# Performance work log

Hardware: AMD Instinct MI355X
Metric: run time of the kernel (lower is better)

## Reference

```python
import jax, jax.numpy as jnp
import numpy as np

N_NODE = 50000
EMB = 128
LAYERS = 2
B = 1024
L = 50
E = 1_600_000


def setup_inputs() -> dict:
    key = jax.random.key(0)
    ks = jax.random.split(key, 21)
    d = EMB
    stdv = 1.0 / np.sqrt(d)
    u = lambda k, shape: jax.random.uniform(k, shape, minval=-stdv, maxval=stdv, dtype=jnp.float32)
    inp = {
        'adj_row': jax.random.randint(ks[0], (E,), 0, N_NODE, dtype=jnp.int32),
        'adj_col': jax.random.randint(ks[1], (E,), 0, N_NODE, dtype=jnp.int32),
        'adj_val': jax.random.uniform(ks[2], (E,), dtype=jnp.float32) / 32.0,  # ~row-normalized sparse adjacency
        'embedding': jax.random.normal(ks[3], (N_NODE, d), dtype=jnp.float32) * 0.1,
        'session_item': jax.random.randint(ks[4], (B, L), 0, N_NODE, dtype=jnp.int32),  # 0 hits the zero pad row
        'session_len': jnp.full((B, 1), float(L), dtype=jnp.float32),
        'D': jax.random.uniform(ks[5], (B, B), dtype=jnp.float32) / B,
        'A_sess': jax.random.uniform(ks[6], (B, B), dtype=jnp.float32) / B,
        'A_gnn': jax.random.uniform(ks[7], (B, L, 2 * L), dtype=jnp.float32) / L,
        'alias_pos': jax.random.randint(ks[8], (B, L), 0, L, dtype=jnp.int32),
        'hidden': jax.random.normal(ks[9], (B, L, d), dtype=jnp.float32) * 0.1,
        'W_in': u(ks[10], (d, d)), 'b_in': u(ks[11], (d,)),
        'W_out': u(ks[12], (d, d)), 'b_out': u(ks[13], (d,)),
        'w_ih': u(ks[14], (3 * d, 2 * d)), 'b_ih': u(ks[15], (3 * d,)),
        'w_hh': u(ks[16], (3 * d, d)), 'b_hh': u(ks[17], (3 * d,)),
        'b_iah': u(ks[18], (d,)), 'b_oah': u(ks[19], (d,)),
    }
    return inp


def reference(adj_row, adj_col, adj_val, embedding, session_item, session_len,
              D, A_sess, A_gnn, alias_pos, hidden,
              W_in, b_in, W_out, b_out, w_ih, b_ih, w_hh, b_hh, b_iah, b_oah):
    # ---- HyperConv: layers of sparse (COO) adjacency @ embedding, summed over hops ----
    emb = embedding
    final = embedding
    for _ in range(LAYERS):
        emb = jax.ops.segment_sum(adj_val[:, None] * emb[adj_col], adj_row, num_segments=N_NODE)
        final = final + emb
    item_emb = final  # [N_NODE, d]

    # ---- LineConv: zero-padded gather + mean pool over session, then session-graph propagation ----
    pad_table = jnp.concatenate([jnp.zeros((1, EMB), embedding.dtype), embedding], axis=0)
    seq_h = pad_table[session_item]                      # [B, L, d]
    sess = jnp.sum(seq_h, axis=1) / session_len          # [B, d]
    DA = D @ A_sess                                      # [B, B]
    acc = sess
    s = sess
    for _ in range(LAYERS):
        s = DA @ s
        acc = acc + s
    session_emb = acc                                    # [B, d]

    # ---- GNN: gather per-session in/out adjacency rows, gated GRU-style update ----
    in_out = jnp.take_along_axis(A_gnn, alias_pos[:, :, None], axis=1)  # [B, L, 2L]
    h_in = hidden @ W_in.T + b_in
    h_out = hidden @ W_out.T + b_out
    input_in = jnp.einsum('bij,bjd->bid', in_out[:, :, :L], h_in) + b_iah
    input_out = jnp.einsum('bij,bjd->bid', in_out[:, :, L:], h_out) + b_oah
    inputs = jnp.concatenate([input_in, input_out], axis=2)             # [B, L, 2d]
    gi = inputs @ w_ih.T + b_ih
    gh = hidden @ w_hh.T + b_hh
    i_r, i_i, i_n = jnp.split(gi, 3, axis=2)
    h_r, h_i, h_n = jnp.split(gh, 3, axis=2)
    resetgate = jax.nn.sigmoid(i_r + h_r)
    inputgate = jax.nn.sigmoid(i_i + h_i)
    newgate = jnp.tanh(i_n + resetgate * h_n)
    hy = newgate + inputgate * (hidden - newgate)        # [B, L, d]

    return item_emb, session_emb, hy
```

## Files before the change

### kernel.cpp

```cpp
#include <hip/hip_runtime.h>

#define EMB 128
#define NN 50000
#define BB 1024
#define LL 50
#define NBK 49
#define NEB 512

typedef float f32x4 __attribute__((ext_vector_type(4)));
typedef float f32x2 __attribute__((ext_vector_type(2)));
typedef unsigned short u16;
typedef unsigned int u32;
typedef unsigned long long u64;
typedef u16 u16x4 __attribute__((ext_vector_type(4)));
typedef u32 u32x4 __attribute__((ext_vector_type(4)));
typedef short bf16x8 __attribute__((ext_vector_type(8)));

__device__ __forceinline__ float u2f(u16 u) {
    union { unsigned int i; float f; } v; v.i = ((unsigned int)u) << 16; return v.f;
}
__device__ __forceinline__ u16 f2b(float f) {
    union { float f; unsigned int i; } v; v.f = f;
    unsigned int i = v.i;
    return (u16)((i + 0x7FFFu + ((i >> 16) & 1u)) >> 16);
}
__device__ __forceinline__ float lo2f(u32 w) { return u2f((u16)(w & 0xffffu)); }
__device__ __forceinline__ float hi2f(u32 w) { return u2f((u16)(w >> 16)); }
__device__ __forceinline__ float sigmoidf_(float x) { return 1.f / (1.f + __expf(-x)); }

__device__ __forceinline__ bf16x8 ld_cvt8(const float* p) {
    f32x4 v0 = *(const f32x4*)p;
    f32x4 v1 = *(const f32x4*)(p + 4);
    union { u16 u[8]; bf16x8 b; } r;
#pragma unroll
    for (int t = 0; t < 4; t++) { r.u[t] = f2b(v0[t]); r.u[4 + t] = f2b(v1[t]); }
    return r.b;
}

__global__ __launch_bounds__(256) void prep_kernel(
    const float* __restrict__ emb, const float* __restrict__ A, const float* __restrict__ D,
    const float* __restrict__ wih, const float* __restrict__ whh,
    const float* __restrict__ Win, const float* __restrict__ Wout,
    u16* __restrict__ emb_bf, u16* __restrict__ A_bf, u16* __restrict__ D_bf,
    u16* __restrict__ wih_bf, u16* __restrict__ whh_bf,
    u16* __restrict__ Win_bf, u16* __restrict__ Wout_bf,
    const int* __restrict__ rowi, int* __restrict__ bcnt,
    int E, int chunk)
{
    __shared__ int lc[NBK];
    int gid = blockIdx.x * 256 + threadIdx.x;
    int stride = gridDim.x * 256;
    int tid = threadIdx.x;
    if (blockIdx.x < NEB) {
        if (tid < NBK) lc[tid] = 0;
        __syncthreads();
        int beg = blockIdx.x * chunk, end = min(E, beg + chunk);
        for (int e = beg + tid; e < end; e += 256)
            atomicAdd(&lc[rowi[e] >> 10], 1);
        __syncthreads();
        if (tid < NBK) bcnt[blockIdx.x * NBK + tid] = lc[tid];
    }
    for (int i = gid; i < 1600000; i += stride) {
        f32x4 v = *(const f32x4*)(emb + (size_t)i * 4);
        u16x4 p;
#pragma unroll
        for (int t = 0; t < 4; t++) p[t] = f2b(v[t]);
        *(u16x4*)(emb_bf + (size_t)i * 4) = p;
    }
    for (int i = gid; i < 2277376; i += stride) {
        const float* s; u16* d; int off;
        if (i < 1048576)      { s = A;    d = A_bf;    off = i; }
        else if (i < 2097152) { s = D;    d = D_bf;    off = i - 1048576; }
        else if (i < 2195456) { s = wih;  d = wih_bf;  off = i - 2097152; }
        else if (i < 2244608) { s = whh;  d = whh_bf;  off = i - 2195456; }
        else if (i < 2260992) { s = Win;  d = Win_bf;  off = i - 2244608; }
        else                  { s = Wout; d = Wout_bf; off = i - 2260992; }
        d[off] = f2b(s[off]);
    }
}

__global__ __launch_bounds__(512) void bktscan_kernel(
    const int* __restrict__ bcnt, int* __restrict__ sofs, int* __restrict__ btot)
{
    __shared__ int ps[512];
    int k = blockIdx.x, t = threadIdx.x;
    int c = bcnt[t * NBK + k];
    ps[t] = c; __syncthreads();
    for (int off = 1; off < 512; off <<= 1) {
        int v = (t >= off) ? ps[t - off] : 0;
        __syncthreads();
        ps[t] += v; __syncthreads();
    }
    sofs[t * NBK + k] = ps[t] - c;
    if (t == 511) btot[k] = ps[511];
}

__global__ __launch_bounds__(64) void btotal_kernel(
    const int* __restrict__ btot, int* __restrict__ bofs, int E)
{
    if (threadIdx.x == 0) {
        int run = 0;
        for (int k = 0; k < NBK; k++) { bofs[k] = run; run += btot[k]; }
        bofs[NBK] = E;
    }
}

__global__ __launch_bounds__(256) void emit_kernel(
    const int* __restrict__ rowi, const int* __restrict__ coli, const float* __restrict__ val,
    const int* __restrict__ sofs, const int* __restrict__ bofs,
    u64* __restrict__ egs, int E, int chunk)
{
    __shared__ int cur[NBK];
    int b = blockIdx.x, tid = threadIdx.x;
    if (tid < NBK) cur[tid] = bofs[tid] + sofs[b * NBK + tid];
    __syncthreads();
    int beg = b * chunk, end = min(E, beg + chunk);
    for (int e = beg + tid; e < end; e += 256) {
        int r = rowi[e];
        int slot = atomicAdd(&cur[r >> 10], 1);
        u64 entry = ((u64)(u32)(r & 1023) << 32)
                  | (u64)((u32)(u16)coli[e] | ((u32)f2b(val[e]) << 16));
        egs[slot] = entry;
    }
}

__global__ __launch_bounds__(1024) void binsort2_kernel(
    const u64* __restrict__ egs, const int* __restrict__ bofs,
    int* __restrict__ row_ptr, u32* __restrict__ eg, int E)
{
    __shared__ int cnt_s[1024];
    __shared__ int ps[1024];
    int k = blockIdx.x, tid = threadIdx.x;
    int r0 = k << 10;
    int beg = bofs[k], end = bofs[k + 1];
    cnt_s[tid] = 0;
    __syncthreads();
    for (int i = beg + tid; i < end; i += 1024)
        atomicAdd(&cnt_s[(int)(egs[i] >> 32)], 1);
    __syncthreads();
    int v = cnt_s[tid];
    ps[tid] = v; __syncthreads();
    for (int off = 1; off < 1024; off <<= 1) {
        int t = (tid >= off) ? ps[tid - off] : 0;
        __syncthreads();
        ps[tid] += t; __syncthreads();
    }
    int ex = beg + ps[tid] - v;
    if (r0 + tid <= NN) row_ptr[r0 + tid] = ex;
    if (k == NBK - 1 && tid == 1023) row_ptr[NN] = E;
    cnt_s[tid] = ex;
    __syncthreads();
    for (int i = beg + tid; i < end; i += 1024) {
        u64 entry = egs[i];
        int rlo = (int)(entry >> 32);
        int p = atomicAdd(&cnt_s[rlo], 1);
        eg[p] = (u32)entry;
    }
}

template<int FUSE>
__global__ __launch_bounds__(256) void gatherb_kernel(
    const int* __restrict__ row_ptr, const u32* __restrict__ eg,
    const u16* __restrict__ src, const float* __restrict__ emb0,
    u16* __restrict__ dst_bf, float* __restrict__ dst_f)
{
    int wave = threadIdx.x >> 6;
    int lane = threadIdx.x & 63;
    int g  = lane >> 4;
    int fl = lane & 15;
    int r = blockIdx.x * 4 + wave;
    if (r >= NN) return;
    int beg = row_ptr[r], end = row_ptr[r + 1];

    float acc[8];
#pragma unroll
    for (int t = 0; t < 8; t++) acc[t] = 0.f;

    if (beg < end) {
        int last = end - 1;
        int npair = (end - beg + 7) >> 3;
        u32 pkA = eg[min(beg + g, last)];
        u32 pkB = eg[min(beg + 4 + g, last)];
        float vA = (beg + g     < end) ? u2f((u16)(pkA >> 16)) : 0.f;
        float vB = (beg + 4 + g < end) ? u2f((u16)(pkB >> 16)) : 0.f;
        u32x4 xA = *(const u32x4*)(src + ((pkA & 0xffffu) << 7) + (fl << 3));
        u32x4 xB = *(const u32x4*)(src + ((pkB & 0xffffu) << 7) + (fl << 3));
        pkA = eg[min(beg + 8  + g, last)];
        pkB = eg[min(beg + 12 + g, last)];

        int e = beg;
        for (int p = 0; p < npair; p++) {
            float cvA = vA, cvB = vB;
            u32x4 cxA = xA, cxB = xB;
            int eN = e + 8;
            vA = (eN + g     < end) ? u2f((u16)(pkA >> 16)) : 0.f;
            vB = (eN + 4 + g < end) ? u2f((u16)(pkB >> 16)) : 0.f;
            xA = *(const u32x4*)(src + ((pkA & 0xffffu) << 7) + (fl << 3));
            xB = *(const u32x4*)(src + ((pkB & 0xffffu) << 7) + (fl << 3));
            int eS = e + 16;
            pkA = eg[min(eS + g, last)];
            pkB = eg[min(eS + 4 + g, last)];
#pragma unroll
            for (int t = 0; t < 4; t++) {
                acc[2 * t]     += cvA * lo2f(cxA[t]);
                acc[2 * t + 1] += cvA * hi2f(cxA[t]);
            }
#pragma unroll
            for (int t = 0; t < 4; t++) {
                acc[2 * t]     += cvB * lo2f(cxB[t]);
                acc[2 * t + 1] += cvB * hi2f(cxB[t]);
            }
            e += 8;
        }
    }

#pragma unroll
    for (int t = 0; t < 8; t++) {
        acc[t] += __shfl_xor(acc[t], 16);
        acc[t] += __shfl_xor(acc[t], 32);
    }

    if (lane < 16) {
        if (FUSE) {
            u32x4 s = *(const u32x4*)(src + ((u32)r << 7) + (lane << 3));
            const float* e0p = emb0 + ((size_t)r << 7) + (lane << 3);
            f32x4 e0a = *(const f32x4*)e0p;
            f32x4 e0b = *(const f32x4*)(e0p + 4);
            f32x4 o0, o1;
#pragma unroll
            for (int t = 0; t < 2; t++) {
                o0[2 * t]     = acc[2 * t]     + e0a[2 * t]     + lo2f(s[t]);
                o0[2 * t + 1] = acc[2 * t + 1] + e0a[2 * t + 1] + hi2f(s[t]);
                o1[2 * t]     = acc[4 + 2 * t]     + e0b[2 * t]     + lo2f(s[2 + t]);
                o1[2 * t + 1] = acc[4 + 2 * t + 1] + e0b[2 * t + 1] + hi2f(s[2 + t]);
            }
            float* dp = dst_f + ((size_t)r << 7) + (lane << 3);
            *(f32x4*)dp = o0;
            *(f32x4*)(dp + 4) = o1;
        } else {
            u32x4 w;
#pragma unroll
            for (int t = 0; t < 4; t++)
                w[t] = (u32)f2b(acc[2 * t]) | ((u32)f2b(acc[2 * t + 1]) << 16);
            *(u32x4*)(dst_bf + ((size_t)r << 7) + (lane << 3)) = w;
        }
    }
}

__global__ __launch_bounds__(128) void sess_pool_kernel(
    const int* __restrict__ items, const float* __restrict__ emb,
    const float* __restrict__ slen, float* __restrict__ sess, u16* __restrict__ sessT)
{
    int b = blockIdx.x, d = threadIdx.x;
    const int* it = items + b * LL;
    float acc = 0.f;
    for (int l = 0; l < LL; l++) {
        int idx = it[l];
        if (idx > 0) acc += emb[(size_t)(idx - 1) * EMB + d];
    }
    float v = acc / slen[b];
    sess[b * EMB + d] = v;
    sessT[d * BB + b] = f2b(v);
}

template<int WT, int WF>
__global__ __launch_bounds__(256) void mm_mfma_kernel(
    const u16* __restrict__ M_bf, const u16* __restrict__ Xt_bf,
    u16* __restrict__ Ct_bf, float* __restrict__ C_f)
{
    int tid = threadIdx.x;
    int wv = tid >> 6, lane = tid & 63, cl = lane & 15, kg = lane >> 4;
    int rbase = blockIdx.x * 16;
    f32x4 acc[2];
    acc[0] = (f32x4)0.f; acc[1] = (f32x4)0.f;
    const u16* arow = M_bf + (size_t)(rbase + cl) * BB + kg * 8;
    const u16* brow = Xt_bf + (size_t)(wv * 32 + cl) * BB + kg * 8;
#pragma unroll 4
    for (int k0 = 0; k0 < BB; k0 += 32) {
        bf16x8 a  = *(const bf16x8*)(arow + k0);
        bf16x8 b0 = *(const bf16x8*)(brow + k0);
        bf16x8 b1 = *(const bf16x8*)(brow + (size_t)16 * BB + k0);
        acc[0] = __builtin_amdgcn_mfma_f32_16x16x32_bf16(a, b0, acc[0], 0, 0, 0);
        acc[1] = __builtin_amdgcn_mfma_f32_16x16x32_bf16(a, b1, acc[1], 0, 0, 0);
    }
#pragma unroll
    for (int nt = 0; nt < 2; nt++) {
        int col = (wv * 2 + nt) * 16 + cl;
#pragma unroll
        for (int j = 0; j < 4; j++) {
            int row = rbase + kg * 4 + j;
            if (WF) C_f[(size_t)row * EMB + col] = acc[nt][j];
            if (WT) Ct_bf[(size_t)col * BB + row] = f2b(acc[nt][j]);
        }
    }
}

__global__ __launch_bounds__(256) void out1_kernel(
    const float* __restrict__ a, const float* __restrict__ b,
    const float* __restrict__ c, float* __restrict__ o, int n)
{
    int i = blockIdx.x * 256 + threadIdx.x;
    if (i < n) o[i] = a[i] + b[i] + c[i];
}

__global__ __launch_bounds__(512) void gnn_tail_kernel(
    const float* __restrict__ hidden,
    const u16* __restrict__ W_in_bf, const u16* __restrict__ W_out_bf,
    const float* __restrict__ b_in, const float* __restrict__ b_out,
    const float* __restrict__ A_gnn, const int* __restrict__ alias_pos,
    const float* __restrict__ b_iah, const float* __restrict__ b_oah,
    const u16* __restrict__ w_ih_bf, const float* __restrict__ b_ih,
    const u16* __restrict__ w_hh_bf, const float* __restrict__ b_hh,
    float* __restrict__ hy)
{
    __shared__ __attribute__((aligned(16))) u16 AioHs[64 * 128];
    __shared__ __attribute__((aligned(16))) u16 hTsXs[256 * 72];
    int b = blockIdx.x;
    int tid = threadIdx.x;
    int wv = tid >> 6, lane = tid & 63, cl = lane & 15, kg = lane >> 4;
    int wr = wv & 3;
    int wh = wv >> 2;

    int pr_row[4], pr_c4[4], ppos[4];
#pragma unroll
    for (int it = 0; it < 4; it++) {
        int i = tid + it * 512;
        pr_row[it] = i >> 5; pr_c4[it] = i & 31;
        ppos[it] = (pr_row[it] < LL) ? alias_pos[b * LL + pr_row[it]] : 0;
    }
    float av[4][4];
#pragma unroll
    for (int it = 0; it < 4; it++) {
        const float* ar = A_gnn + ((size_t)b * LL + ppos[it]) * (2 * LL);
#pragma unroll
        for (int t = 0; t < 4; t++) {
            int jp = pr_c4[it] * 4 + t;
            int col = (jp < 64) ? jp : (50 + (jp - 64));
            int ok = (pr_row[it] < LL) && ((jp < 64) ? (jp < LL) : ((jp - 64) < LL));
            av[it][t] = ok ? ar[col] : 0.f;
        }
    }

    {
        const float* hsrc = hidden + (size_t)b * LL * EMB;
        int mr = wr * 16 + cl;
        const u16* wsrc = wh ? W_out_bf : W_in_bf;
        f32x4 acc1[8];
#pragma unroll
        for (int nt = 0; nt < 8; nt++) acc1[nt] = (f32x4)0.f;
#pragma unroll
        for (int ks = 0; ks < 4; ks++) {
            int k0 = ks * 32;
            bf16x8 a = (mr < LL) ? ld_cvt8(hsrc + mr * 128 + k0 + kg * 8) : (bf16x8)0;
#pragma unroll
            for (int nt = 0; nt < 8; nt++) {
                int wrow = nt * 16 + cl;
                bf16x8 bf = *(const bf16x8*)(wsrc + (size_t)wrow * 128 + k0 + kg * 8);
                acc1[nt] = __builtin_amdgcn_mfma_f32_16x16x32_bf16(a, bf, acc1[nt], 0, 0, 0);
            }
        }
#pragma unroll
        for (int nt = 0; nt < 8; nt++) {
            int col = (wh * 8 + nt) * 16 + cl;
            float bias = (col < 128) ? b_in[col] : b_out[col - 128];
            int r0 = wr * 16 + kg * 4;
            u16x4 p;
#pragma unroll
            for (int j = 0; j < 4; j++)
                p[j] = (r0 + j < LL) ? f2b(acc1[nt][j] + bias) : (u16)0;
            *(u16x4*)&hTsXs[col * 72 + r0] = p;
        }
    }

#pragma unroll
    for (int it = 0; it < 4; it++) {
        u16x4 p;
#pragma unroll
        for (int t = 0; t < 4; t++) p[t] = f2b(av[it][t]);
        *(u16x4*)((char*)AioHs + pr_row[it] * 256 + ((pr_c4[it] * 8) ^ ((pr_row[it] & 7) << 4))) = p;
    }
    __syncthreads();

    f32x4 acc[8];
#pragma unroll
    for (int nt = 0; nt < 8; nt++) acc[nt] = (f32x4)0.f;
#pragma unroll
    for (int ks = 0; ks < 2; ks++) {
#pragma unroll
        for (int nt8 = 0; nt8 < 8; nt8++) {
            int nt = wh * 8 + nt8;
            int k0 = wh * 64 + ks * 32;
            int mr = wr * 16 + cl;
            bf16x8 a = *(const bf16x8*)((const char*)AioHs + mr * 256 +
                        (((k0 << 1) + (kg << 4)) ^ ((mr & 7) << 4)));
            bf16x8 bf = *(const bf16x8*)&hTsXs[(nt * 16 + cl) * 72 + ks * 32 + kg * 8];
            acc[nt8] = __builtin_amdgcn_mfma_f32_16x16x32_bf16(a, bf, acc[nt8], 0, 0, 0);
        }
    }
    __syncthreads();

#pragma unroll
    for (int nt8 = 0; nt8 < 8; nt8++) {
        int dp = (wh * 8 + nt8) * 16 + cl;
        float bias = (dp < 128) ? b_iah[dp] : b_oah[dp - 128];
#pragma unroll
        for (int j = 0; j < 4; j++) {
            int i = wr * 16 + kg * 4 + j;
            *(u16*)((char*)hTsXs + i * 512 + ((dp * 2) ^ ((i & 7) << 4))) =
                f2b(acc[nt8][j] + bias);
        }
    }
    {
        const float* hsrc = hidden + (size_t)b * LL * EMB;
#pragma unroll
        for (int i2 = 0; i2 < 4; i2++) {
            int lin = i2 * 512 + tid;
            int row = lin >> 5, c4 = lin & 31;
            u16x4 p = (u16x4)0;
            if (row < LL) {
                f32x4 v = *(const f32x4*)(hsrc + row * 128 + c4 * 4);
#pragma unroll
                for (int t = 0; t < 4; t++) p[t] = f2b(v[t]);
            }
            *(u16x4*)((char*)AioHs + row * 256 + ((c4 * 8) ^ ((row & 7) << 4))) = p;
        }
    }
    __syncthreads();

    f32x4 acc_ri[4][2];
    f32x4 acc_n1[4];
    f32x4 acc_n2[4];
#pragma unroll
    for (int mt = 0; mt < 4; mt++) {
        acc_ri[mt][0] = (f32x4)0.f; acc_ri[mt][1] = (f32x4)0.f;
        acc_n1[mt] = (f32x4)0.f; acc_n2[mt] = (f32x4)0.f;
    }

#pragma unroll
    for (int ks = 0; ks < 8; ks++) {
        int k0 = ks * 32;
        bf16x8 a[4];
#pragma unroll
        for (int mt = 0; mt < 4; mt++) {
            int mr = mt * 16 + cl;
            a[mt] = *(const bf16x8*)((const char*)hTsXs + mr * 512 +
                     (((k0 << 1) + (kg << 4)) ^ ((mr & 7) << 4)));
        }
#pragma unroll
        for (int g = 0; g < 3; g++) {
            int brow = g * 128 + wv * 16 + cl;
            bf16x8 bw = *(const bf16x8*)(w_ih_bf + (size_t)brow * 256 + k0 + kg * 8);
#pragma unroll
            for (int mt = 0; mt < 4; mt++) {
                f32x4* dst = (g < 2) ? &acc_ri[mt][g] : &acc_n1[mt];
                *dst = __builtin_amdgcn_mfma_f32_16x16x32_bf16(a[mt], bw, *dst, 0, 0, 0);
            }
        }
    }
#pragma unroll
    for (int ks = 0; ks < 4; ks++) {
        int k0 = ks * 32;
        bf16x8 a[4];
#pragma unroll
        for (int mt = 0; mt < 4; mt++) {
            int mr = mt * 16 + cl;
            a[mt] = *(const bf16x8*)((const char*)AioHs + mr * 256 +
                     (((k0 << 1) + (kg << 4)) ^ ((mr & 7) << 4)));
        }
#pragma unroll
        for (int g = 0; g < 3; g++) {
            int brow = g * 128 + wv * 16 + cl;
            bf16x8 bw = *(const bf16x8*)(w_hh_bf + (size_t)brow * 128 + k0 + kg * 8);
#pragma unroll
            for (int mt = 0; mt < 4; mt++) {
                f32x4* dst = (g < 2) ? &acc_ri[mt][g] : &acc_n2[mt];
                *dst = __builtin_amdgcn_mfma_f32_16x16x32_bf16(a[mt], bw, *dst, 0, 0, 0);
            }
        }
    }

    {
        int d = wv * 16 + cl;
        float br = b_ih[d] + b_hh[d];
        float bi = b_ih[128 + d] + b_hh[128 + d];
        float bn1 = b_ih[256 + d], bn2 = b_hh[256 + d];
#pragma unroll
        for (int mt = 0; mt < 4; mt++)
#pragma unroll
            for (int j = 0; j < 4; j++) {
                int row = mt * 16 + kg * 4 + j;
                if (row >= LL) continue;
                float rg = sigmoidf_(acc_ri[mt][0][j] + br);
                float ig = sigmoidf_(acc_ri[mt][1][j] + bi);
                float ng = tanhf(acc_n1[mt][j] + bn1 + rg * (acc_n2[mt][j] + bn2));
                u16 hb = *(const u16*)((const char*)AioHs + row * 256 + ((d * 2) ^ ((row & 7) << 4)));
                float h = u2f(hb);
                hy[((size_t)b * LL + row) * 128 + d] = ng + ig * (h - ng);
            }
    }
}

extern "C" void kernel_launch(void* const* d_in, const int* in_sizes, int n_in,
                              void* d_out, int out_size, void* d_ws, size_t ws_size,
                              hipStream_t stream) {
    (void)n_in; (void)out_size; (void)ws_size;
    const int*   adj_row      = (const int*)d_in[0];
    const int*   adj_col      = (const int*)d_in[1];
    const float* adj_val      = (const float*)d_in[2];
    const float* embedding    = (const float*)d_in[3];
    const int*   session_item = (const int*)d_in[4];
    const float* session_len  = (const float*)d_in[5];
    const float* Dm           = (const float*)d_in[6];
    const float* A_sess       = (const float*)d_in[7];
    const float* A_gnn        = (const float*)d_in[8];
    const int*   alias_pos    = (const int*)d_in[9];
    const float* hidden       = (const float*)d_in[10];
    const float* W_in         = (const float*)d_in[11];
    const float* b_in         = (const float*)d_in[12];
    const float* W_out        = (const float*)d_in[13];
    const float* b_out        = (const float*)d_in[14];
    const float* w_ih         = (const float*)d_in[15];
    const float* b_ih         = (const float*)d_in[16];
    const float* w_hh         = (const float*)d_in[17];
    const float* b_hh         = (const float*)d_in[18];
    const float* b_iah        = (const float*)d_in[19];
    const float* b_oah        = (const float*)d_in[20];
    const int E = in_sizes[0];

    float* out0 = (float*)d_out;
    float* out1 = out0 + 6400000;
    float* out2 = out1 + 131072;

    float* ws = (float*)d_ws;
    u16*  emb_bf  = (u16*)ws;
    int*  bcnt  = (int*)(ws + 3200000);
    int*  sofs  = (int*)(ws + 3230000);
    int*  btot  = (int*)(ws + 3260000);
    u16*  accA_bf = (u16*)(ws + 3200000);
    u32*  eg    = (u32*)(ws + 6400000);
    u64*  egs   = (u64*)(ws + 8000000);
    float* sess  = ws + 11200000;
    u16*   sessT = (u16*)(ws + 11350000);
    u16*   t1T   = (u16*)(ws + 11400000);
    u16*   s1T   = (u16*)(ws + 11450000);
    u16*   t2T   = (u16*)(ws + 11500000);
    float* s1    = ws + 11550000;
    float* s2    = ws + 11700000;
    u16*   A_bf  = (u16*)(ws + 11850000);
    u16*   D_bf  = (u16*)(ws + 12400000);
    int*   row_ptr = (int*)(ws + 12950000);
    int*   bofs    = row_ptr + NN + 1;
    u16* w_ih_bf   = (u16*)(ws + 13107200);
    u16* w_hh_bf   = w_ih_bf + 98304;
    u16* W_in_bf   = w_hh_bf + 49152;
    u16* W_out_bf  = W_in_bf + 16384;

    int chunk = (E + NEB - 1) / NEB;

    prep_kernel<<<2048, 256, 0, stream>>>(embedding, A_sess, Dm, w_ih, w_hh, W_in, W_out,
                                          emb_bf, A_bf, D_bf, w_ih_bf, w_hh_bf, W_in_bf, W_out_bf,
                                          adj_row, bcnt, E, chunk);

    bktscan_kernel<<<NBK, 512, 0, stream>>>(bcnt, sofs, btot);
    btotal_kernel<<<1, 64, 0, stream>>>(btot, bofs, E);
    emit_kernel<<<NEB, 256, 0, stream>>>(adj_row, adj_col, adj_val, sofs, bofs, egs, E, chunk);
    binsort2_kernel<<<NBK, 1024, 0, stream>>>(egs, bofs, row_ptr, eg, E);
    gatherb_kernel<0><<<(NN + 3) / 4, 256, 0, stream>>>(row_ptr, eg, emb_bf, embedding, accA_bf, (float*)nullptr);
    gatherb_kernel<1><<<(NN + 3) / 4, 256, 0, stream>>>(row_ptr, eg, accA_bf, embedding, (u16*)nullptr, out0);

    sess_pool_kernel<<<BB, 128, 0, stream>>>(session_item, embedding, session_len, sess, sessT);
    mm_mfma_kernel<1, 0><<<64, 256, 0, stream>>>(A_bf, sessT, t1T, (float*)nullptr);
    mm_mfma_kernel<1, 1><<<64, 256, 0, stream>>>(D_bf, t1T, s1T, s1);
    mm_mfma_kernel<1, 0><<<64, 256, 0, stream>>>(A_bf, s1T, t2T, (float*)nullptr);
    mm_mfma_kernel<0, 1><<<64, 256, 0, stream>>>(D_bf, t2T, (u16*)nullptr, s2);
    out1_kernel<<<(131072 + 255) / 256, 256, 0, stream>>>(sess, s1, s2, out1, 131072);

    gnn_tail_kernel<<<BB, 512, 0, stream>>>(hidden, W_in_bf, W_out_bf, b_in, b_out,
                                            A_gnn, alias_pos, b_iah, b_oah,
                                            w_ih_bf, b_ih, w_hh_bf, b_hh, out2);
}
```

Measured before the change: 327.5 us.

## Fold W_in/W_out into w_ih weights and reassociate GNN input projection

Reassociates the GNN branch so that the per-session adjacency multiplies the raw hidden state first (A·H). The result then goes through a precombined weight w_ih·[W_in;W_out], built once per call by a small kernel. The bias terms are folded into per-row correction vectors scaled by the adjacency row sums. This drops the per-block H·W_in/W_out GEMM and the intermediate bias pass in the tail kernel. In exchange it adds two small precompute kernels, and bf16 rounding now falls at different points.

```diff
diff --git a/kernel.cpp b/kernel.cpp
--- a/kernel.cpp
+++ b/kernel.cpp
@@ -28,22 +28,11 @@
 __device__ __forceinline__ float hi2f(u32 w) { return u2f((u16)(w >> 16)); }
 __device__ __forceinline__ float sigmoidf_(float x) { return 1.f / (1.f + __expf(-x)); }
 
-__device__ __forceinline__ bf16x8 ld_cvt8(const float* p) {
-    f32x4 v0 = *(const f32x4*)p;
-    f32x4 v1 = *(const f32x4*)(p + 4);
-    union { u16 u[8]; bf16x8 b; } r;
-#pragma unroll
-    for (int t = 0; t < 4; t++) { r.u[t] = f2b(v0[t]); r.u[4 + t] = f2b(v1[t]); }
-    return r.b;
-}
-
 __global__ __launch_bounds__(256) void prep_kernel(
     const float* __restrict__ emb, const float* __restrict__ A, const float* __restrict__ D,
-    const float* __restrict__ wih, const float* __restrict__ whh,
-    const float* __restrict__ Win, const float* __restrict__ Wout,
+    const float* __restrict__ whh,
     u16* __restrict__ emb_bf, u16* __restrict__ A_bf, u16* __restrict__ D_bf,
-    u16* __restrict__ wih_bf, u16* __restrict__ whh_bf,
-    u16* __restrict__ Win_bf, u16* __restrict__ Wout_bf,
+    u16* __restrict__ whh_bf,
     const int* __restrict__ rowi, int* __restrict__ bcnt,
     int E, int chunk)
 {
@@ -67,16 +56,47 @@
         for (int t = 0; t < 4; t++) p[t] = f2b(v[t]);
         *(u16x4*)(emb_bf + (size_t)i * 4) = p;
     }
-    for (int i = gid; i < 2277376; i += stride) {
+    for (int i = gid; i < 2146304; i += stride) {
         const float* s; u16* d; int off;
-        if (i < 1048576)      { s = A;    d = A_bf;    off = i; }
-        else if (i < 2097152) { s = D;    d = D_bf;    off = i - 1048576; }
-        else if (i < 2195456) { s = wih;  d = wih_bf;  off = i - 2097152; }
-        else if (i < 2244608) { s = whh;  d = whh_bf;  off = i - 2195456; }
-        else if (i < 2260992) { s = Win;  d = Win_bf;  off = i - 2244608; }
-        else                  { s = Wout; d = Wout_bf; off = i - 2260992; }
+        if (i < 1048576)      { s = A;   d = A_bf;   off = i; }
+        else if (i < 2097152) { s = D;   d = D_bf;   off = i - 1048576; }
+        else                  { s = whh; d = whh_bf; off = i - 2097152; }
         d[off] = f2b(s[off]);
     }
+}
+
+__global__ __launch_bounds__(256) void wcomb_kernel(
+    const float* __restrict__ w_ih, const float* __restrict__ W_in, const float* __restrict__ W_out,
+    u16* __restrict__ WcT_bf)
+{
+    __shared__ float wrow[256];
+    int d = blockIdx.x, c = threadIdx.x;
+    wrow[c] = w_ih[d * 256 + c];
+    __syncthreads();
+    const float* W = (c < 128) ? W_in : W_out;
+    const float* wr = wrow + ((c < 128) ? 0 : 128);
+    int cc = c & 127;
+    float acc = 0.f;
+#pragma unroll 4
+    for (int j = 0; j < 128; j++) acc += wr[j] * W[j * 128 + cc];
+    WcT_bf[d * 256 + c] = f2b(acc);
+}
+
+__global__ __launch_bounds__(384) void u123_kernel(
+    const float* __restrict__ w_ih, const float* __restrict__ b_in, const float* __restrict__ b_out,
+    const float* __restrict__ b_iah, const float* __restrict__ b_oah, const float* __restrict__ b_ih,
+    float* __restrict__ u123)
+{
+    int d = threadIdx.x;
+    float a1 = 0.f, a2 = 0.f, a3 = 0.f;
+#pragma unroll 4
+    for (int j = 0; j < 128; j++) {
+        float wl = w_ih[d * 256 + j], wh = w_ih[d * 256 + 128 + j];
+        a1 += b_in[j] * wl;
+        a2 += b_out[j] * wh;
+        a3 += b_iah[j] * wl + b_oah[j] * wh;
+    }
+    u123[d] = a1; u123[384 + d] = a2; u123[768 + d] = a3 + b_ih[d];
 }
 
 __global__ __launch_bounds__(512) void bktscan_kernel(
@@ -305,21 +325,21 @@
 
 __global__ __launch_bounds__(512) void gnn_tail_kernel(
     const float* __restrict__ hidden,
-    const u16* __restrict__ W_in_bf, const u16* __restrict__ W_out_bf,
-    const float* __restrict__ b_in, const float* __restrict__ b_out,
     const float* __restrict__ A_gnn, const int* __restrict__ alias_pos,
-    const float* __restrict__ b_iah, const float* __restrict__ b_oah,
-    const u16* __restrict__ w_ih_bf, const float* __restrict__ b_ih,
-    const u16* __restrict__ w_hh_bf, const float* __restrict__ b_hh,
+    const u16* __restrict__ WcT_bf, const u16* __restrict__ w_hh_bf,
+    const float* __restrict__ u123, const float* __restrict__ b_hh,
     float* __restrict__ hy)
 {
-    __shared__ __attribute__((aligned(16))) u16 AioHs[64 * 128];
-    __shared__ __attribute__((aligned(16))) u16 hTsXs[256 * 72];
+    __shared__ __attribute__((aligned(16))) u16 smem[24576];
+    u16* Hs  = smem;
+    u16* As  = smem + 8192;
+    u16* HsT = smem + 16384;
+    u16* M2s = smem + 8192;
+    __shared__ float rcs[64][2];
+
     int b = blockIdx.x;
     int tid = threadIdx.x;
     int wv = tid >> 6, lane = tid & 63, cl = lane & 15, kg = lane >> 4;
-    int wr = wv & 3;
-    int wh = wv >> 2;
 
     int pr_row[4], pr_c4[4], ppos[4];
 #pragma unroll
@@ -340,90 +360,84 @@
             av[it][t] = ok ? ar[col] : 0.f;
         }
     }
-
-    {
-        const float* hsrc = hidden + (size_t)b * LL * EMB;
-        int mr = wr * 16 + cl;
-        const u16* wsrc = wh ? W_out_bf : W_in_bf;
-        f32x4 acc1[8];
-#pragma unroll
-        for (int nt = 0; nt < 8; nt++) acc1[nt] = (f32x4)0.f;
-#pragma unroll
-        for (int ks = 0; ks < 4; ks++) {
-            int k0 = ks * 32;
-            bf16x8 a = (mr < LL) ? ld_cvt8(hsrc + mr * 128 + k0 + kg * 8) : (bf16x8)0;
-#pragma unroll
-            for (int nt = 0; nt < 8; nt++) {
-                int wrow = nt * 16 + cl;
-                bf16x8 bf = *(const bf16x8*)(wsrc + (size_t)wrow * 128 + k0 + kg * 8);
-                acc1[nt] = __builtin_amdgcn_mfma_f32_16x16x32_bf16(a, bf, acc1[nt], 0, 0, 0);
-            }
-        }
-#pragma unroll
-        for (int nt = 0; nt < 8; nt++) {
-            int col = (wh * 8 + nt) * 16 + cl;
-            float bias = (col < 128) ? b_in[col] : b_out[col - 128];
-            int r0 = wr * 16 + kg * 4;
-            u16x4 p;
-#pragma unroll
-            for (int j = 0; j < 4; j++)
-                p[j] = (r0 + j < LL) ? f2b(acc1[nt][j] + bias) : (u16)0;
-            *(u16x4*)&hTsXs[col * 72 + r0] = p;
-        }
-    }
-
+    const float* hsrc = hidden + (size_t)b * LL * EMB;
+    f32x4 hv[4]; int hrow[4], hc4[4];
+#pragma unroll
+    for (int i2 = 0; i2 < 4; i2++) {
+        int lin = i2 * 512 + tid;
+        hrow[i2] = lin >> 5; hc4[i2] = lin & 31;
+        hv[i2] = (hrow[i2] < LL) ? *(const f32x4*)(hsrc + hrow[i2] * 128 + hc4[i2] * 4) : (f32x4)0.f;
+    }
 #pragma unroll
     for (int it = 0; it < 4; it++) {
         u16x4 p;
 #pragma unroll
         for (int t = 0; t < 4; t++) p[t] = f2b(av[it][t]);
-        *(u16x4*)((char*)AioHs + pr_row[it] * 256 + ((pr_c4[it] * 8) ^ ((pr_row[it] & 7) << 4))) = p;
-    }
-    __syncthreads();
-
-    f32x4 acc[8];
-#pragma unroll
-    for (int nt = 0; nt < 8; nt++) acc[nt] = (f32x4)0.f;
-#pragma unroll
-    for (int ks = 0; ks < 2; ks++) {
-#pragma unroll
-        for (int nt8 = 0; nt8 < 8; nt8++) {
-            int nt = wh * 8 + nt8;
-            int k0 = wh * 64 + ks * 32;
-            int mr = wr * 16 + cl;
-            bf16x8 a = *(const bf16x8*)((const char*)AioHs + mr * 256 +
-                        (((k0 << 1) + (kg << 4)) ^ ((mr & 7) << 4)));
-            bf16x8 bf = *(const bf16x8*)&hTsXs[(nt * 16 + cl) * 72 + ks * 32 + kg * 8];
-            acc[nt8] = __builtin_amdgcn_mfma_f32_16x16x32_bf16(a, bf, acc[nt8], 0, 0, 0);
-        }
-    }
-    __syncthreads();
-
-#pragma unroll
-    for (int nt8 = 0; nt8 < 8; nt8++) {
-        int dp = (wh * 8 + nt8) * 16 + cl;
-        float bias = (dp < 128) ? b_iah[dp] : b_oah[dp - 128];
-#pragma unroll
-        for (int j = 0; j < 4; j++) {
-            int i = wr * 16 + kg * 4 + j;
-            *(u16*)((char*)hTsXs + i * 512 + ((dp * 2) ^ ((i & 7) << 4))) =
-                f2b(acc[nt8][j] + bias);
-        }
-    }
+        *(u16x4*)((char*)As + pr_row[it] * 256 + ((pr_c4[it] * 8) ^ ((pr_row[it] & 7) << 4))) = p;
+    }
+#pragma unroll
+    for (int i2 = 0; i2 < 4; i2++) {
+        u16x4 q;
+#pragma unroll
+        for (int t = 0; t < 4; t++) q[t] = f2b(hv[i2][t]);
+        *(u16x4*)((char*)Hs + hrow[i2] * 256 + ((hc4[i2] * 8) ^ ((hrow[i2] & 7) << 4))) = q;
+#pragma unroll
+        for (int t = 0; t < 4; t++) {
+            int c = hc4[i2] * 4 + t;
+            *(u16*)((char*)HsT + c * 128 + ((hrow[i2] * 2) ^ ((c & 7) << 4))) = q[t];
+        }
+    }
+    __syncthreads();
+
+    if (tid < 128) {
+        int row = tid >> 1, half = tid & 1;
+        float s = 0.f;
+#pragma unroll
+        for (int c4 = 0; c4 < 16; c4++) {
+            u16x4 v = *(const u16x4*)((const char*)As + row * 256 +
+                        ((half * 128 + c4 * 8) ^ ((row & 7) << 4)));
+            s += u2f(v[0]) + u2f(v[1]) + u2f(v[2]) + u2f(v[3]);
+        }
+        rcs[row][half] = s;
+    }
+
     {
-        const float* hsrc = hidden + (size_t)b * LL * EMB;
-#pragma unroll
-        for (int i2 = 0; i2 < 4; i2++) {
-            int lin = i2 * 512 + tid;
-            int row = lin >> 5, c4 = lin & 31;
-            u16x4 p = (u16x4)0;
-            if (row < LL) {
-                f32x4 v = *(const f32x4*)(hsrc + row * 128 + c4 * 4);
-#pragma unroll
-                for (int t = 0; t < 4; t++) p[t] = f2b(v[t]);
-            }
-            *(u16x4*)((char*)AioHs + row * 256 + ((c4 * 8) ^ ((row & 7) << 4))) = p;
-        }
+        int h = wv >> 2, ct = wv & 3;
+        f32x4 m2acc[4][2];
+#pragma unroll
+        for (int mt = 0; mt < 4; mt++) { m2acc[mt][0] = (f32x4)0.f; m2acc[mt][1] = (f32x4)0.f; }
+#pragma unroll
+        for (int ks = 0; ks < 2; ks++) {
+            bf16x8 bb[2];
+#pragma unroll
+            for (int nt = 0; nt < 2; nt++) {
+                int c = ct * 32 + nt * 16 + cl;
+                bb[nt] = *(const bf16x8*)((const char*)HsT + c * 128 +
+                          ((ks * 64 + kg * 16) ^ ((c & 7) << 4)));
+            }
+#pragma unroll
+            for (int mt = 0; mt < 4; mt++) {
+                int mr = mt * 16 + cl;
+                bf16x8 aa = *(const bf16x8*)((const char*)As + mr * 256 +
+                             ((h * 128 + ks * 64 + kg * 16) ^ ((mr & 7) << 4)));
+#pragma unroll
+                for (int nt = 0; nt < 2; nt++)
+                    m2acc[mt][nt] = __builtin_amdgcn_mfma_f32_16x16x32_bf16(aa, bb[nt], m2acc[mt][nt], 0, 0, 0);
+            }
+        }
+        __syncthreads();
+#pragma unroll
+        for (int mt = 0; mt < 4; mt++)
+#pragma unroll
+            for (int nt = 0; nt < 2; nt++) {
+                int kcol = h * 128 + ct * 32 + nt * 16 + cl;
+#pragma unroll
+                for (int j = 0; j < 4; j++) {
+                    int row = mt * 16 + kg * 4 + j;
+                    *(u16*)((char*)M2s + row * 512 + ((kcol * 2) ^ ((row & 7) << 4))) =
+                        f2b(m2acc[mt][nt][j]);
+                }
+            }
     }
     __syncthreads();
 
@@ -438,18 +452,17 @@
 
 #pragma unroll
     for (int ks = 0; ks < 8; ks++) {
-        int k0 = ks * 32;
         bf16x8 a[4];
 #pragma unroll
         for (int mt = 0; mt < 4; mt++) {
             int mr = mt * 16 + cl;
-            a[mt] = *(const bf16x8*)((const char*)hTsXs + mr * 512 +
-                     (((k0 << 1) + (kg << 4)) ^ ((mr & 7) << 4)));
+            a[mt] = *(const bf16x8*)((const char*)M2s + mr * 512 +
+                     ((ks * 64 + kg * 16) ^ ((mr & 7) << 4)));
         }
 #pragma unroll
         for (int g = 0; g < 3; g++) {
             int brow = g * 128 + wv * 16 + cl;
-            bf16x8 bw = *(const bf16x8*)(w_ih_bf + (size_t)brow * 256 + k0 + kg * 8);
+            bf16x8 bw = *(const bf16x8*)(WcT_bf + (size_t)brow * 256 + ks * 32 + kg * 8);
 #pragma unroll
             for (int mt = 0; mt < 4; mt++) {
                 f32x4* dst = (g < 2) ? &acc_ri[mt][g] : &acc_n1[mt];
@@ -459,18 +472,17 @@
     }
 #pragma unroll
     for (int ks = 0; ks < 4; ks++) {
-        int k0 = ks * 32;
         bf16x8 a[4];
 #pragma unroll
         for (int mt = 0; mt < 4; mt++) {
             int mr = mt * 16 + cl;
-            a[mt] = *(const bf16x8*)((const char*)AioHs + mr * 256 +
-                     (((k0 << 1) + (kg << 4)) ^ ((mr & 7) << 4)));
+            a[mt] = *(const bf16x8*)((const char*)Hs + mr * 256 +
+                     ((ks * 64 + kg * 16) ^ ((mr & 7) << 4)));
         }
 #pragma unroll
         for (int g = 0; g < 3; g++) {
             int brow = g * 128 + wv * 16 + cl;
-            bf16x8 bw = *(const bf16x8*)(w_hh_bf + (size_t)brow * 128 + k0 + kg * 8);
+            bf16x8 bw = *(const bf16x8*)(w_hh_bf + (size_t)brow * 128 + ks * 32 + kg * 8);
 #pragma unroll
             for (int mt = 0; mt < 4; mt++) {
                 f32x4* dst = (g < 2) ? &acc_ri[mt][g] : &acc_n2[mt];
@@ -481,19 +493,25 @@
 
     {
         int d = wv * 16 + cl;
-        float br = b_ih[d] + b_hh[d];
-        float bi = b_ih[128 + d] + b_hh[128 + d];
-        float bn1 = b_ih[256 + d], bn2 = b_hh[256 + d];
+        float brh = b_hh[d], bih_ = b_hh[128 + d], bnh = b_hh[256 + d];
+        float u1r = u123[d],       u1i = u123[128 + d],       u1n = u123[256 + d];
+        float u2r = u123[384 + d], u2i = u123[384 + 128 + d], u2n = u123[384 + 256 + d];
+        float u3r = u123[768 + d], u3i = u123[768 + 128 + d], u3n = u123[768 + 256 + d];
 #pragma unroll
         for (int mt = 0; mt < 4; mt++)
 #pragma unroll
             for (int j = 0; j < 4; j++) {
                 int row = mt * 16 + kg * 4 + j;
                 if (row >= LL) continue;
-                float rg = sigmoidf_(acc_ri[mt][0][j] + br);
-                float ig = sigmoidf_(acc_ri[mt][1][j] + bi);
-                float ng = tanhf(acc_n1[mt][j] + bn1 + rg * (acc_n2[mt][j] + bn2));
-                u16 hb = *(const u16*)((const char*)AioHs + row * 256 + ((d * 2) ^ ((row & 7) << 4)));
+                float cr = rcs[row][0], dr = rcs[row][1];
+                float pr  = acc_ri[mt][0][j] + cr * u1r + dr * u2r + u3r + brh;
+                float pi  = acc_ri[mt][1][j] + cr * u1i + dr * u2i + u3i + bih_;
+                float pn1 = acc_n1[mt][j]    + cr * u1n + dr * u2n + u3n;
+                float pn2 = acc_n2[mt][j] + bnh;
+                float rg = sigmoidf_(pr);
+                float ig = sigmoidf_(pi);
+                float ng = tanhf(pn1 + rg * pn2);
+                u16 hb = *(const u16*)((const char*)Hs + row * 256 + ((d * 2) ^ ((row & 7) << 4)));
                 float h = u2f(hb);
                 hy[((size_t)b * LL + row) * 128 + d] = ng + ig * (h - ng);
             }
@@ -550,16 +568,17 @@
     u16*   D_bf  = (u16*)(ws + 12400000);
     int*   row_ptr = (int*)(ws + 12950000);
     int*   bofs    = row_ptr + NN + 1;
-    u16* w_ih_bf   = (u16*)(ws + 13107200);
-    u16* w_hh_bf   = w_ih_bf + 98304;
-    u16* W_in_bf   = w_hh_bf + 49152;
-    u16* W_out_bf  = W_in_bf + 16384;
+    u16* WcT_bf    = (u16*)(ws + 13107200);
+    u16* w_hh_bf   = WcT_bf + 98304;
+    float* u123    = (float*)(w_hh_bf + 49152);
 
     int chunk = (E + NEB - 1) / NEB;
 
-    prep_kernel<<<2048, 256, 0, stream>>>(embedding, A_sess, Dm, w_ih, w_hh, W_in, W_out,
-                                          emb_bf, A_bf, D_bf, w_ih_bf, w_hh_bf, W_in_bf, W_out_bf,
+    prep_kernel<<<2048, 256, 0, stream>>>(embedding, A_sess, Dm, w_hh,
+                                          emb_bf, A_bf, D_bf, w_hh_bf,
                                           adj_row, bcnt, E, chunk);
+    wcomb_kernel<<<384, 256, 0, stream>>>(w_ih, W_in, W_out, WcT_bf);
+    u123_kernel<<<1, 384, 0, stream>>>(w_ih, b_in, b_out, b_iah, b_oah, b_ih, u123);
 
     bktscan_kernel<<<NBK, 512, 0, stream>>>(bcnt, sofs, btot);
     btotal_kernel<<<1, 64, 0, stream>>>(btot, bofs, E);
@@ -575,7 +594,6 @@
     mm_mfma_kernel<0, 1><<<64, 256, 0, stream>>>(D_bf, t2T, (u16*)nullptr, s2);
     out1_kernel<<<(131072 + 255) / 256, 256, 0, stream>>>(sess, s1, s2, out1, 131072);
 
-    gnn_tail_kernel<<<BB, 512, 0, stream>>>(hidden, W_in_bf, W_out_bf, b_in, b_out,
-                                            A_gnn, alias_pos, b_iah, b_oah,
-                                            w_ih_bf, b_ih, w_hh_bf, b_hh, out2);
-}
+    gnn_tail_kernel<<<BB, 512, 0, stream>>>(hidden, A_gnn, alias_pos,
+                                            WcT_bf, w_hh_bf, u123, b_hh, out2);
+}
```

After: 340.0 us. 1.04x slower.
